# Kernel tuning notes

Hardware: AMD Instinct MI355X
Metric: run time of the kernel (lower is better)

## Reference

```python
import jax, jax.numpy as jnp
import numpy as np

N, IN_DIM, LAT, NB = 4096, 3000, 64, 2
SINKHORN_ITERS = 3


def _bce_logits(x, y):
    # torch BCEWithLogitsLoss, mean reduction, numerically stable
    return jnp.mean(jnp.maximum(x, 0.0) - x * y + jnp.log1p(jnp.exp(-jnp.abs(x))))


def _forward(feature_set, adj_set, graph_neigh_set, label_CSL_set, dist_mat_set,
             enc_W, dec_W, Ms, disc_W, disc_b, perm_idx):
    nb = feature_set.shape[0]
    hs = []
    loss_sl = 0.0
    loss_feat = 0.0
    for k in range(nb):  # small fixed loop over slices
        x, adj, mask, lab = feature_set[k], adj_set[k], graph_neigh_set[k], label_CSL_set[k]
        h = adj @ (x @ enc_W[k])            # GCN encode: spmm(adj, x @ W)
        out = adj @ (h @ dec_W[k])          # GCN decode
        x_a = x[perm_idx[k]]                # permutation(x): row shuffle
        h_a = adj @ (x_a @ enc_W[k])
        hr, har = jax.nn.relu(h), jax.nn.relu(h_a)

        def readout(emb):
            vsum = mask @ emb
            ge = vsum / mask.sum(1, keepdims=True)
            nrm = jnp.linalg.norm(ge, axis=1, keepdims=True)
            return ge / jnp.maximum(nrm, 1e-12)   # F.normalize p=2

        g = jax.nn.sigmoid(readout(hr))
        g_a = jax.nn.sigmoid(readout(har))

        def disc(c, hp, hm):
            s1 = jnp.einsum('nd,de,ne->n', hp, disc_W, c) + disc_b[0]
            s2 = jnp.einsum('nd,de,ne->n', hm, disc_W, c) + disc_b[0]
            return jnp.stack([s1, s2], axis=1)  # [N,2]

        ret = disc(g, hr, har)
        ret_a = disc(g_a, har, hr)
        loss_sl = loss_sl + _bce_logits(ret, lab) + _bce_logits(ret_a, lab)
        loss_feat = loss_feat + jnp.mean((x - out) ** 2)
        hs.append(h)

    loss_align = 0.0; loss_align_fix = 0.0; loss_maintain = 0.0
    loss_marginal = 0.0; loss_sparsity = 0.0
    for k in range(1, nb):
        src, tgt = hs[k - 1], hs[k]
        M = Ms[k - 1]
        m1, m2 = src.shape[0], tgt.shape[0]
        C = (src @ M) @ (tgt @ M).T / jnp.sqrt(jnp.float32(M.shape[0]))
        P = jax.nn.softmax(C, axis=1) / m1
        # NonSquareSinkhornKnopp.fit: alternate row/col normalization to uniform marginals
        for _ in range(SINKHORN_ITERS):
            P = P / (m1 * P.sum(1, keepdims=True))
            P = P / (m2 * P.sum(0, keepdims=True))
        cxy = P / P.sum(1, keepdims=True)
        cyx = P.T / P.T.sum(1, keepdims=True)
        # cdist(src, tgt)
        d2 = jnp.sum(src ** 2, 1)[:, None] + jnp.sum(tgt ** 2, 1)[None, :] - 2.0 * (src @ tgt.T)
        cd = jnp.sqrt(jnp.maximum(d2, 1e-12))
        loss_align = loss_align + jnp.sum(P * cd)
        f0, f1 = feature_set[k - 1], feature_set[k]
        loss_align_fix = loss_align_fix + jnp.mean((f0 - cxy @ f1) ** 2) + jnp.mean((f1 - cyx @ f0) ** 2)
        D0, D1 = dist_mat_set[k - 1], dist_mat_set[k]
        diff1 = D0 - cxy @ (D1 @ cxy.T)
        diff2 = D1 - cyx @ (D0 @ cyx.T)
        loss_maintain = loss_maintain + jnp.linalg.norm(diff1) / m1 + jnp.linalg.norm(diff2) / m2
        # replicate torch F.kl_div(input, target) = mean(target*(log target - input))
        p = jnp.full((m2,), 1.0 / m2, jnp.float32)
        q = P.sum(0)
        kld_pq = jnp.mean(q * (jnp.log(q) - p))
        kld_pp = jnp.mean(p * (jnp.log(p) - p))
        loss_marginal = loss_marginal + (kld_pq - kld_pp) * m2
        loss_sparsity = loss_sparsity - jnp.sum(P * jnp.log(P + 1e-10))
    return jnp.stack([loss_sl, loss_feat, loss_align, loss_align_fix,
                      loss_maintain, loss_marginal, loss_sparsity])


def setup_inputs():
    key = jax.random.key(0)
    ks = jax.random.split(key, 12)
    feature_set = jax.random.normal(ks[0], (NB, N, IN_DIM), jnp.float32)
    A = jax.random.uniform(ks[1], (NB, N, N), jnp.float32)
    adj_set = A / A.sum(-1, keepdims=True)  # row-stochastic dense stand-in for normalized sparse adj
    mask = (jax.random.uniform(ks[2], (NB, N, N)) < 0.01).astype(jnp.float32)
    graph_neigh_set = mask + jnp.eye(N, dtype=jnp.float32)[None]  # nonzero row sums
    lab = jnp.concatenate([jnp.ones((N, 1)), jnp.zeros((N, 1))], axis=1).astype(jnp.float32)
    label_CSL_set = jnp.broadcast_to(lab, (NB, N, 2))
    D = jax.random.uniform(ks[3], (NB, N, N), jnp.float32)
    dist_mat_set = 0.5 * (D + jnp.swapaxes(D, 1, 2))
    perm_idx = jnp.stack([jax.random.permutation(ks[4 + i], N) for i in range(NB)]).astype(jnp.int32)
    s_enc = np.float32(np.sqrt(2.0 / (IN_DIM + LAT)))
    enc_W = jax.random.normal(ks[6], (NB, IN_DIM, LAT), jnp.float32) * s_enc
    dec_W = jax.random.normal(ks[7], (NB, LAT, IN_DIM), jnp.float32) * s_enc
    s_lat = np.float32(np.sqrt(1.0 / LAT))
    Ms = jax.random.normal(ks[8], (NB - 1, LAT, LAT), jnp.float32) * s_lat
    disc_W = jax.random.normal(ks[9], (LAT, LAT), jnp.float32) * s_lat
    disc_b = jnp.zeros((1,), jnp.float32)
    return dict(feature_set=feature_set, adj_set=adj_set, graph_neigh_set=graph_neigh_set,
                label_CSL_set=label_CSL_set, dist_mat_set=dist_mat_set, perm_idx=perm_idx,
                enc_W=enc_W, dec_W=dec_W, Ms=Ms, disc_W=disc_W, disc_b=disc_b)


def reference(feature_set, adj_set, graph_neigh_set, label_CSL_set, dist_mat_set,
              perm_idx, enc_W, dec_W, Ms, disc_W, disc_b):
    return _forward(feature_set, adj_set, graph_neigh_set, label_CSL_set, dist_mat_set,
                    enc_W, dec_W, Ms, disc_W, disc_b, perm_idx)
```

## Files before the change

kernel.cpp:

```cpp
#include <hip/hip_runtime.h>
#include <cmath>

constexpr int kN   = 4096;
constexpr int kIN  = 3000;
constexpr int kINp = 3072;
constexpr int kLAT = 64;

enum { SL = 0, FEAT, ALN, FXA, FXB, SM1, SM2, SPS, NSLOT };

typedef __bf16 bf16x8 __attribute__((ext_vector_type(8)));
typedef float f32x4 __attribute__((ext_vector_type(4)));
typedef unsigned short u16x8 __attribute__((ext_vector_type(8)));
typedef unsigned short u16x4 __attribute__((ext_vector_type(4)));

template<bool IS_MAX>
__device__ __forceinline__ float blk_red(float v) {
  __shared__ float buf[4];
  #pragma unroll
  for (int s = 32; s > 0; s >>= 1) {
    float o = __shfl_down(v, s, 64);
    v = IS_MAX ? fmaxf(v, o) : (v + o);
  }
  int lane = threadIdx.x & 63, wv = threadIdx.x >> 6, nw = blockDim.x >> 6;
  __syncthreads();
  if (lane == 0) buf[wv] = v;
  __syncthreads();
  float r = buf[0];
  for (int i = 1; i < nw; i++) r = IS_MAX ? fmaxf(r, buf[i]) : (r + buf[i]);
  return r;
}

__device__ __forceinline__ float wave_red_sum(float v) {
  #pragma unroll
  for (int s = 32; s > 0; s >>= 1) v += __shfl_down(v, s, 64);
  return v;
}

__device__ __forceinline__ unsigned short f2bf(float f) {
  unsigned u = __builtin_bit_cast(unsigned, f);
  u += 0x7fffu + ((u >> 16) & 1u);
  return (unsigned short)(u >> 16);
}
__device__ __forceinline__ float bf2f(unsigned short h) {
  return __builtin_bit_cast(float, (unsigned)h << 16);
}

__device__ __forceinline__ void gload16(const unsigned short* g, unsigned short* l) {
  __builtin_amdgcn_global_load_lds(
      (const __attribute__((address_space(1))) unsigned int*)g,
      (__attribute__((address_space(3))) unsigned int*)l, 16, 0, 0);
}

template<int EPI, int XBF>
__global__ __launch_bounds__(256)
void bt_mfma_k(const unsigned short* __restrict__ A, const unsigned short* __restrict__ Bt,
               unsigned short* __restrict__ Cb, float* __restrict__ Cf,
               const void* __restrict__ Xv,
               const float* __restrict__ rowdiv, const float* __restrict__ coldiv,
               float* __restrict__ slot, int gx, int Nc, int K, int ldX, int sym)
{
  __shared__ unsigned short AB[3 * 8192];

  int orig = blockIdx.x;
  int bx, by;
  if (EPI == 2 && sym) {
    int x = orig & 7, i = orig >> 3;
    int u = x * 66 + i;
    float disc = 4225.f - 8.f * (float)u;
    by = (int)((65.f - sqrtf(fmaxf(disc, 0.f))) * 0.5f);
    while (by > 0 && 32 * by - by * (by - 1) / 2 > u) by--;
    while (32 * (by + 1) - (by + 1) * by / 2 <= u) by++;
    bx = by + (u - (32 * by - by * (by - 1) / 2));
  } else {
    int x = orig & 7, tt = orig >> 3;
    bx = tt >> 2;
    by = x * 4 + (tt & 3);
  }
  const int row0 = by * 128, col0 = bx * 128;

  const int t = threadIdx.x, l = t & 63, wv = t >> 6;
  const int wr = wv >> 1, wc = wv & 1;
  const int lr = l & 15, lkh = (l >> 4) << 3;

  f32x4 acc[4][4];
  #pragma unroll
  for (int i = 0; i < 4; i++)
    #pragma unroll
    for (int j = 0; j < 4; j++) acc[i][j] = (f32x4){0.f, 0.f, 0.f, 0.f};

  const int srow = l >> 2;
  const int sk   = (l & 3) << 3;
  const unsigned short* Ab = A  + (size_t)(row0 + srow) * K + sk;
  const unsigned short* Bb = Bt + (size_t)(col0 + srow) * K + sk;

  const int NT = K >> 5;

  auto STAGE = [&](int kt, int buf) {
    unsigned short* As = AB + buf * 8192;
    unsigned short* Bs = As + 4096;
    int k0 = kt << 5;
    #pragma unroll
    for (int h2 = 0; h2 < 2; h2++) {
      int c = wv * 2 + h2;
      gload16(Ab + (size_t)c * 16 * K + k0, As + c * 512);
      gload16(Bb + (size_t)c * 16 * K + k0, Bs + c * 512);
    }
  };

  STAGE(0, 0);
  if (NT > 1) STAGE(1, 1);
  if (NT > 2) STAGE(2, 2);
  int cur = 0;

  for (int kt = 0; kt < NT; ++kt) {
    int ahead = NT - 1 - kt;
    if (ahead >= 2)      { asm volatile("s_waitcnt vmcnt(8)" ::: "memory"); }
    else if (ahead == 1) { asm volatile("s_waitcnt vmcnt(4)" ::: "memory"); }
    else                 { asm volatile("s_waitcnt vmcnt(0)" ::: "memory"); }
    __builtin_amdgcn_sched_barrier(0);
    __builtin_amdgcn_s_barrier();

    const unsigned short* As = AB + cur * 8192;
    const unsigned short* Bs = As + 4096;
    u16x8 af[4], bfv[4];
    #pragma unroll
    for (int mi = 0; mi < 4; mi++)
      af[mi] = *(const u16x8*)&As[(wr * 64 + mi * 16 + lr) * 32 + lkh];
    #pragma unroll
    for (int ni = 0; ni < 4; ni++)
      bfv[ni] = *(const u16x8*)&Bs[(wc * 64 + ni * 16 + lr) * 32 + lkh];
    #pragma unroll
    for (int mi = 0; mi < 4; mi++)
      #pragma unroll
      for (int ni = 0; ni < 4; ni++)
        acc[mi][ni] = __builtin_amdgcn_mfma_f32_16x16x32_bf16(
            __builtin_bit_cast(bf16x8, af[mi]),
            __builtin_bit_cast(bf16x8, bfv[ni]), acc[mi][ni], 0, 0, 0);

    __builtin_amdgcn_s_barrier();
    if (kt + 3 < NT) STAGE(kt + 3, cur);
    cur = (cur == 2) ? 0 : cur + 1;
  }

  const int lcol = l & 15, lrow = (l >> 4) << 2;
  if (EPI == 0) {
    #pragma unroll
    for (int mi = 0; mi < 4; mi++) {
      int rr = row0 + wr * 64 + mi * 16 + lrow;
      #pragma unroll
      for (int ni = 0; ni < 4; ni++) {
        int cc = col0 + wc * 64 + ni * 16 + lcol;
        #pragma unroll
        for (int r = 0; r < 4; r++) {
          float v = acc[mi][ni][r];
          if (rowdiv) v /= rowdiv[rr + r];
          Cb[(size_t)(rr + r) * 4096 + cc] = f2bf(v);
        }
      }
    }
  } else if (EPI == 1) {
    #pragma unroll
    for (int mi = 0; mi < 4; mi++) {
      int rr = row0 + wr * 64 + mi * 16 + lrow;
      #pragma unroll
      for (int ni = 0; ni < 4; ni++) {
        int cc = col0 + wc * 64 + ni * 16 + lcol;
        #pragma unroll
        for (int r = 0; r < 4; r++)
          Cf[(size_t)(rr + r) * 4096 + cc] = acc[mi][ni][r];
      }
    }
  } else if (EPI == 2) {
    const float* Xf = (const float*)Xv;
    const unsigned short* Xh = (const unsigned short*)Xv;
    float part = 0.f;
    #pragma unroll
    for (int mi = 0; mi < 4; mi++) {
      int rr = row0 + wr * 64 + mi * 16 + lrow;
      #pragma unroll
      for (int ni = 0; ni < 4; ni++) {
        int cc = col0 + wc * 64 + ni * 16 + lcol;
        if (cc < Nc) {
          float cd = coldiv ? coldiv[cc] : 1.f;
          #pragma unroll
          for (int r = 0; r < 4; r++) {
            float v = acc[mi][ni][r];
            if (rowdiv) v /= rowdiv[rr + r];
            v /= cd;
            size_t xi = (size_t)(rr + r) * ldX + cc;
            float xval = XBF ? bf2f(Xh[xi]) : Xf[xi];
            float d = xval - v;
            part = fmaf(d, d, part);
          }
        }
      }
    }
    part = blk_red<false>(part);
    if (t == 0) {
      float wgt = (sym && col0 > row0) ? 2.f : 1.f;
      atomicAdd(slot, part * wgt);
    }
  } else {
    const unsigned short* Ph = (const unsigned short*)Xv;
    float a = 0.f, sp = 0.f;
    #pragma unroll
    for (int mi = 0; mi < 4; mi++) {
      int rr = row0 + wr * 64 + mi * 16 + lrow;
      #pragma unroll
      for (int ni = 0; ni < 4; ni++) {
        int cc = col0 + wc * 64 + ni * 16 + lcol;
        #pragma unroll
        for (int r = 0; r < 4; r++) {
          float g = acc[mi][ni][r];
          float p = bf2f(Ph[(size_t)(rr + r) * ldX + cc]);
          float d2 = rowdiv[rr + r] + coldiv[cc] - 2.f * g;
          a = fmaf(p, sqrtf(fmaxf(d2, 1e-12f)), a);
          sp = fmaf(p, logf(p + 1e-10f), sp);
        }
      }
    }
    a = blk_red<false>(a);
    sp = blk_red<false>(sp);
    if (t == 0) { atomicAdd(&slot[ALN], a); atomicAdd(&slot[SPS], sp); }
  }
}

__global__ __launch_bounds__(256)
void ns_mfma_k(const unsigned short* __restrict__ A, const unsigned short* __restrict__ Bt,
               float* __restrict__ C, int Nc, int K, int KC, int ldC)
{
  __shared__ unsigned short AB[2 * 8192];
  int ks = blockIdx.x & 15, strip = blockIdx.x >> 4;
  const int row0 = strip * 128;
  const int kbase = ks * KC;

  const int t = threadIdx.x, l = t & 63, wv = t >> 6;
  const int wr = wv >> 1, wc = wv & 1;
  const int lr = l & 15, lkh = (l >> 4) << 3;

  f32x4 acc[4][4];
  #pragma unroll
  for (int i = 0; i < 4; i++)
    #pragma unroll
    for (int j = 0; j < 4; j++) acc[i][j] = (f32x4){0.f, 0.f, 0.f, 0.f};

  const int srow = l >> 2;
  const int sk   = (l & 3) << 3;
  const unsigned short* Ab = A  + (size_t)(row0 + srow) * K + kbase + sk;
  const unsigned short* Bb = Bt + (size_t)srow * K + kbase + sk;

  const int NT = KC >> 5;

  auto STAGE = [&](int kt, int buf) {
    unsigned short* As = AB + buf * 8192;
    unsigned short* Bs = As + 4096;
    int k0 = kt << 5;
    #pragma unroll
    for (int h2 = 0; h2 < 2; h2++) {
      int c = wv * 2 + h2;
      gload16(Ab + (size_t)c * 16 * K + k0, As + c * 512);
      gload16(Bb + (size_t)c * 16 * K + k0, Bs + c * 512);
    }
  };

  STAGE(0, 0);
  if (NT > 1) STAGE(1, 1);
  int cur = 0;

  for (int kt = 0; kt < NT; ++kt) {
    if (kt + 1 < NT) { asm volatile("s_waitcnt vmcnt(4)" ::: "memory"); }
    else             { asm volatile("s_waitcnt vmcnt(0)" ::: "memory"); }
    __builtin_amdgcn_sched_barrier(0);
    __builtin_amdgcn_s_barrier();

    const unsigned short* As = AB + cur * 8192;
    const unsigned short* Bs = As + 4096;
    u16x8 af[4], bfv[4];
    #pragma unroll
    for (int mi = 0; mi < 4; mi++)
      af[mi] = *(const u16x8*)&As[(wr * 64 + mi * 16 + lr) * 32 + lkh];
    #pragma unroll
    for (int ni = 0; ni < 4; ni++)
      bfv[ni] = *(const u16x8*)&Bs[(wc * 64 + ni * 16 + lr) * 32 + lkh];
    #pragma unroll
    for (int mi = 0; mi < 4; mi++)
      #pragma unroll
      for (int ni = 0; ni < 4; ni++)
        acc[mi][ni] = __builtin_amdgcn_mfma_f32_16x16x32_bf16(
            __builtin_bit_cast(bf16x8, af[mi]),
            __builtin_bit_cast(bf16x8, bfv[ni]), acc[mi][ni], 0, 0, 0);

    __builtin_amdgcn_s_barrier();
    if (kt + 2 < NT) STAGE(kt + 2, cur);
    cur ^= 1;
  }

  const int lcol = l & 15, lrow = (l >> 4) << 2;
  #pragma unroll
  for (int mi = 0; mi < 4; mi++) {
    int rr = row0 + wr * 64 + mi * 16 + lrow;
    #pragma unroll
    for (int ni = 0; ni < 4; ni++) {
      int cc = wc * 64 + ni * 16 + lcol;
      if (cc < Nc) {
        #pragma unroll
        for (int r = 0; r < 4; r++)
          atomicAdd(&C[(size_t)(rr + r) * ldC + cc], acc[mi][ni][r]);
      }
    }
  }
}

__global__ void cvt_k(const float* __restrict__ s, unsigned short* __restrict__ d,
                      int n8, float scale)
{
  int i = blockIdx.x * 256 + threadIdx.x;
  if (i < n8) {
    float4 a = ((const float4*)s)[2 * i], b = ((const float4*)s)[2 * i + 1];
    u16x8 w;
    w[0] = f2bf(a.x * scale); w[1] = f2bf(a.y * scale);
    w[2] = f2bf(a.z * scale); w[3] = f2bf(a.w * scale);
    w[4] = f2bf(b.x * scale); w[5] = f2bf(b.y * scale);
    w[6] = f2bf(b.z * scale); w[7] = f2bf(b.w * scale);
    ((u16x8*)d)[i] = w;
  }
}

__global__ void cvt_pad_k(const float* __restrict__ s, unsigned short* __restrict__ d)
{
  int i = blockIdx.x * 256 + threadIdx.x;
  int row = i / 384, c8 = (i - row * 384) * 8;
  u16x8 w = (u16x8)0;
  if (c8 < kIN) {
    const float* sp = s + (size_t)row * kIN + c8;
    float4 a = *(const float4*)sp, b = *(const float4*)(sp + 4);
    w[0] = f2bf(a.x); w[1] = f2bf(a.y); w[2] = f2bf(a.z); w[3] = f2bf(a.w);
    w[4] = f2bf(b.x); w[5] = f2bf(b.y); w[6] = f2bf(b.z); w[7] = f2bf(b.w);
  }
  ((u16x8*)d)[i] = w;
}

__global__ void cvt_cols_k(const float* __restrict__ s, unsigned short* __restrict__ d)
{
  int i = blockIdx.x * 256 + threadIdx.x;
  int row = i >> 3, c8 = (i & 7) * 8;
  const float* sp = s + (size_t)row * 128 + c8;
  float4 a = *(const float4*)sp, b = *(const float4*)(sp + 4);
  u16x8 w;
  w[0] = f2bf(a.x); w[1] = f2bf(a.y); w[2] = f2bf(a.z); w[3] = f2bf(a.w);
  w[4] = f2bf(b.x); w[5] = f2bf(b.y); w[6] = f2bf(b.z); w[7] = f2bf(b.w);
  ((u16x8*)d)[i] = w;
}

template<bool RELU>
__global__ void tr_k(const float* __restrict__ src, unsigned short* __restrict__ dst,
                     int R, int C, int sld, int dld)
{
  __shared__ float tile[32][33];
  int c0 = blockIdx.x * 32, r0 = blockIdx.y * 32;
  int tr_ = threadIdx.x >> 3, tc4 = (threadIdx.x & 7) << 2;
  #pragma unroll
  for (int j = 0; j < 4; j++) {
    int r = r0 + tr_, c = c0 + tc4 + j;
    float v = (r < R && c < C) ? src[(size_t)r * sld + c] : 0.f;
    if (RELU) v = fmaxf(v, 0.f);
    tile[tr_][tc4 + j] = v;
  }
  __syncthreads();
  u16x4 wv;
  #pragma unroll
  for (int j = 0; j < 4; j++) wv[j] = f2bf(tile[tc4 + j][tr_]);
  *(u16x4*)&dst[(size_t)(c0 + tr_) * dld + r0 + tc4] = wv;
}

__global__ __launch_bounds__(256)
void gemm_small_k(const float* __restrict__ A, const float* __restrict__ B,
                  float* __restrict__ C, int M, int Nc, int K,
                  int ldA, int ldB, int ldC)
{
  __shared__ float As[16][68];
  __shared__ float Bs[16][68];
  int tid = threadIdx.x;
  int tx = tid & 15, ty = tid >> 4;
  int row0 = blockIdx.y * 64, col0 = blockIdx.x * 64;
  float acc[4][4] = {};

  for (int k0 = 0; k0 < K; k0 += 16) {
    {
      int m = tid >> 2, kk = (tid & 3) << 2;
      const float* ap = A + (size_t)(row0 + m) * ldA + k0 + kk;
      float4 v = *(const float4*)ap;
      As[kk + 0][m] = v.x; As[kk + 1][m] = v.y; As[kk + 2][m] = v.z; As[kk + 3][m] = v.w;
    }
    {
      int kk = tid >> 4, c = (tid & 15) << 2;
      const float* bp = B + (size_t)(k0 + kk) * ldB + col0 + c;
      #pragma unroll
      for (int i = 0; i < 4; i++)
        Bs[kk][c + i] = (col0 + c + i < Nc) ? bp[i] : 0.f;
    }
    __syncthreads();
    #pragma unroll
    for (int kk = 0; kk < 16; kk++) {
      float4 a4 = *(const float4*)&As[kk][ty << 2];
      float4 b4 = *(const float4*)&Bs[kk][tx << 2];
      float av[4] = {a4.x, a4.y, a4.z, a4.w};
      float bv[4] = {b4.x, b4.y, b4.z, b4.w};
      #pragma unroll
// ... 24 lines not shown
  int r0 = blockIdx.x * 8;
  float csl[16] = {};
  float cdiv[16];
  if (mode != 0) {
    #pragma unroll
    for (int t = 0; t < 4; t++) {
      float4 c4 = ((const float4*)cs_in)[tid + t * 256];
      cdiv[4 * t + 0] = 1.f / (4096.f * c4.x);
      cdiv[4 * t + 1] = 1.f / (4096.f * c4.y);
      cdiv[4 * t + 2] = 1.f / (4096.f * c4.z);
      cdiv[4 * t + 3] = 1.f / (4096.f * c4.w);
    }
  }
  for (int rr = 0; rr < 8; rr++) {
    int row = r0 + rr;
    float4* prow = (float4*)(P + (size_t)row * 4096);
    float4 r[4];
    #pragma unroll
    for (int t = 0; t < 4; t++) r[t] = prow[tid + t * 256];

    if (mode == 0) {
      float m = -3.4e38f;
      #pragma unroll
      for (int t = 0; t < 4; t++)
        m = fmaxf(m, fmaxf(fmaxf(r[t].x, r[t].y), fmaxf(r[t].z, r[t].w)));
      m = blk_red<true>(m);
      float s = 0.f;
      #pragma unroll
      for (int t = 0; t < 4; t++) {
        r[t].x = expf(r[t].x - m); r[t].y = expf(r[t].y - m);
        r[t].z = expf(r[t].z - m); r[t].w = expf(r[t].w - m);
        s += r[t].x + r[t].y + r[t].z + r[t].w;
      }
      s = blk_red<false>(s);
      float f = 1.f / (s * 4096.f);
      #pragma unroll
      for (int t = 0; t < 4; t++) {
        r[t].x *= f; r[t].y *= f; r[t].z *= f; r[t].w *= f;
        prow[tid + t * 256] = r[t];
        csl[4 * t + 0] += r[t].x; csl[4 * t + 1] += r[t].y;
        csl[4 * t + 2] += r[t].z; csl[4 * t + 3] += r[t].w;
      }
    } else {
      float s = 0.f;
      #pragma unroll
      for (int t = 0; t < 4; t++) {
        r[t].x *= cdiv[4 * t + 0]; r[t].y *= cdiv[4 * t + 1];
        r[t].z *= cdiv[4 * t + 2]; r[t].w *= cdiv[4 * t + 3];
        s += r[t].x + r[t].y + r[t].z + r[t].w;
      }
      s = blk_red<false>(s);
      if (mode == 1) {
        float f = 1.f / (4096.f * s);
        #pragma unroll
        for (int t = 0; t < 4; t++) {
          r[t].x *= f; r[t].y *= f; r[t].z *= f; r[t].w *= f;
          prow[tid + t * 256] = r[t];
          csl[4 * t + 0] += r[t].x; csl[4 * t + 1] += r[t].y;
          csl[4 * t + 2] += r[t].z; csl[4 * t + 3] += r[t].w;
        }
      } else {
        if (tid == 0) rs[row] = s;
        #pragma unroll
        for (int t = 0; t < 4; t++) {
          prow[tid + t * 256] = r[t];
          u16x4 w;
          w[0] = f2bf(r[t].x); w[1] = f2bf(r[t].y);
          w[2] = f2bf(r[t].z); w[3] = f2bf(r[t].w);
          *(u16x4*)&Pb[(size_t)row * 4096 + 4 * (tid + t * 256)] = w;
          csl[4 * t + 0] += r[t].x; csl[4 * t + 1] += r[t].y;
          csl[4 * t + 2] += r[t].z; csl[4 * t + 3] += r[t].w;
        }
      }
    }
  }
  #pragma unroll
  for (int t = 0; t < 4; t++) {
    int j = 4 * (tid + t * 256);
    atomicAdd(&cs_out[j + 0], csl[4 * t + 0]);
    atomicAdd(&cs_out[j + 1], csl[4 * t + 1]);
    atomicAdd(&cs_out[j + 2], csl[4 * t + 2]);
    atomicAdd(&cs_out[j + 3], csl[4 * t + 3]);
  }
}

__global__ __launch_bounds__(256)
void rowsum_k(const float* __restrict__ Pm, float* __restrict__ vec)
{
  int i = blockIdx.x, tid = threadIdx.x;
  const float4* prow = (const float4*)(Pm + (size_t)i * kN);
  float s = 0.f;
  #pragma unroll
  for (int t = 0; t < 4; t++) {
    float4 r = prow[tid + t * 256];
    s += r.x + r.y + r.z + r.w;
  }
  s = blk_red<false>(s);
  if (tid == 0) vec[i] = s;
}

__global__ void relu_k(const float* __restrict__ in, float* __restrict__ out, int n)
{
  int i = blockIdx.x * blockDim.x + threadIdx.x;
  if (i < n) out[i] = fmaxf(in[i], 0.f);
}

__global__ void gather_k(float* __restrict__ XP, const int* __restrict__ perm)
{
  int gid = blockIdx.x * 256 + threadIdx.x;
  int i = gid >> 6, j = gid & 63;
  XP[(size_t)i * 128 + 64 + j] = XP[(size_t)perm[i] * 128 + j];
}

__global__ void sqnorm_k(const float* __restrict__ H, int ld, float* __restrict__ outv)
{
  int gid = blockIdx.x * 256 + threadIdx.x;
  int row = gid >> 6, j = gid & 63;
  float v = H[(size_t)row * ld + j];
  float p = wave_red_sum(v * v);
  if (j == 0) outv[row] = p;
}

__global__ void readout_k(const float* __restrict__ vs2, const float* __restrict__ mrs,
                          float* __restrict__ g2)
{
  int q = blockIdx.x, j = threadIdx.x;
  float v = vs2[(size_t)q * 64 + j] / mrs[q >> 1];
  float p = v * v;
  #pragma unroll
  for (int s = 1; s < 64; s <<= 1) p += __shfl_xor(p, s, 64);
  float nrm = sqrtf(p);
  v = v / fmaxf(nrm, 1e-12f);
  g2[(size_t)q * 64 + j] = 1.f / (1.f + expf(-v));
}

__device__ __forceinline__ float bce_term(float x, float y) {
  return fmaxf(x, 0.f) - x * y + log1pf(expf(-fabsf(x)));
}

__global__ void disc_k(const float* __restrict__ G2, const float* __restrict__ W2,
                       const float* __restrict__ lab, const float* __restrict__ bptr,
                       float* __restrict__ acc)
{
  int i = blockIdx.x, j = threadIdx.x;
  float gj  = G2[(size_t)(2 * i) * 64 + j];
  float gaj = G2[(size_t)(2 * i + 1) * 64 + j];
  float hw  = W2[(size_t)(2 * i) * 64 + j];
  float haw = W2[(size_t)(2 * i + 1) * 64 + j];
  float s1 = hw * gj, s2 = haw * gj, s1a = haw * gaj, s2a = hw * gaj;
  #pragma unroll
  for (int s = 1; s < 64; s <<= 1) {
    s1  += __shfl_xor(s1, s, 64);
    s2  += __shfl_xor(s2, s, 64);
    s1a += __shfl_xor(s1a, s, 64);
    s2a += __shfl_xor(s2a, s, 64);
  }
  if (j == 0) {
    float b = bptr[0];
    float y0 = lab[i * 2 + 0], y1 = lab[i * 2 + 1];
    float t = bce_term(s1 + b, y0) + bce_term(s2 + b, y1)
            + bce_term(s1a + b, y0) + bce_term(s2a + b, y1);
    atomicAdd(&acc[SL], t);
  }
}

__global__ __launch_bounds__(256)
void finalize_k(const float* __restrict__ acc, const float* __restrict__ cs,
                float* __restrict__ out)
{
  int tid = threadIdx.x;
  float invm2 = 1.f / (float)kN;
  float t = 0.f;
  for (int j = tid; j < kN; j += 256) {
    float q = cs[j];
    t += q * (logf(q) - invm2);
  }
  t = blk_red<false>(t);
  if (tid == 0) {
    float kld_pq = t * invm2;
    float kld_pp = invm2 * (logf(invm2) - invm2);
    out[0] = acc[SL] / (2.f * (float)kN);
// ... 23 lines not shown
  const float* discW = (const float*)d_in[9];
  const float* discb = (const float*)d_in[10];
  float* out = (float*)d_out;

  const size_t SZNN = (size_t)kN * kN;

  char* cur = (char*)d_ws;
  auto alloc = [&](size_t bytes) {
    char* p = cur;
    cur += (bytes + 255) & ~(size_t)255;
    return p;
  };
  float* P            = (float*)alloc(SZNN * 4);
  unsigned short* Pb  = (unsigned short*)alloc(SZNN * 2);
  unsigned short* PbT = (unsigned short*)alloc(SZNN * 2);
  unsigned short* Db  = (unsigned short*)alloc(SZNN * 2);
  unsigned short* ajb = (unsigned short*)alloc(SZNN * 2);
  unsigned short* xb  = (unsigned short*)alloc((size_t)kN * kINp * 2);
  unsigned short* dWtb= (unsigned short*)alloc((size_t)kINp * kLAT * 2);
  unsigned short* ahb = (unsigned short*)alloc((size_t)kN * kLAT * 2);
  unsigned short* encWtp = (unsigned short*)alloc((size_t)128 * kINp * 2);
  unsigned short* XPt = (unsigned short*)alloc((size_t)128 * kN * 2);
  unsigned short* hbTp= (unsigned short*)alloc((size_t)128 * kN * 2);
  unsigned short* HRt = (unsigned short*)alloc((size_t)128 * kN * 2);
  unsigned short* smb = (unsigned short*)alloc((size_t)kN * kLAT * 2);
  unsigned short* tmb = (unsigned short*)alloc((size_t)kN * kLAT * 2);
  unsigned short* h0b = (unsigned short*)alloc((size_t)kN * kLAT * 2);
  unsigned short* h1b = (unsigned short*)alloc((size_t)kN * kLAT * 2);
  float* XP  = (float*)alloc((size_t)kN * 128 * 4);
  float* HH0 = (float*)alloc((size_t)kN * 128 * 4);
  float* HH1 = (float*)alloc((size_t)kN * 128 * 4);
  float* HR  = (float*)alloc((size_t)kN * 128 * 4);
  float* VS  = (float*)alloc((size_t)kN * 128 * 4);
  float* G2  = (float*)alloc((size_t)kN * 128 * 4);
  float* W2  = (float*)alloc((size_t)kN * 128 * 4);
  float* SM_ = (float*)alloc((size_t)kN * kLAT * 4);
  float* TM_ = (float*)alloc((size_t)kN * kLAT * 4);
  float* ah  = (float*)alloc((size_t)kN * kLAT * 4);
  float* sns = (float*)alloc(kN * 4);
  float* snt = (float*)alloc(kN * 4);
  float* rs  = (float*)alloc(kN * 4);
  float* cs  = (float*)alloc(kN * 4);
  float* csA = (float*)alloc(kN * 4);
  float* csB = (float*)alloc(kN * 4);
  float* mrs = (float*)alloc(kN * 4);
  float* acc = (float*)alloc(NSLOT * 4);

  unsigned short* Tb  = (unsigned short*)P;
  unsigned short* ftb = ajb;

  hipMemsetAsync(acc, 0, NSLOT * sizeof(float), stream);

  for (int k = 0; k < 2; k++) {
    const float* x    = feat  + (size_t)k * kN * kIN;
    const float* adj  = adjs  + (size_t)k * SZNN;
    const float* msk  = gmask + (size_t)k * SZNN;
    const float* lab  = labs  + (size_t)k * kN * 2;
    const int*   perm = perms + (size_t)k * kN;
    const float* eW   = encW  + (size_t)k * kIN * kLAT;
    const float* dW   = decW  + (size_t)k * kLAT * kIN;
    float* HHk = (k == 0) ? HH0 : HH1;

    cvt_pad_k<<<6144, 256, 0, stream>>>(x, xb);
    hipMemsetAsync(encWtp, 0, (size_t)128 * kINp * 2, stream);
    tr_k<false><<<dim3(2, (kIN + 31) / 32), 256, 0, stream>>>(eW, encWtp, kIN, kLAT, kLAT, kINp);
    hipMemsetAsync(XP, 0, (size_t)kN * 128 * 4, stream);
    ns_mfma_k<<<512, 256, 0, stream>>>(xb, encWtp, XP, kLAT, kINp, kINp / 16, 128);
    gather_k<<<kN * 64 / 256, 256, 0, stream>>>(XP, perm);
    tr_k<false><<<dim3(4, 128), 256, 0, stream>>>(XP, XPt, kN, 128, 128, kN);
    cvt_k<<<(int)(SZNN / 8 / 256), 256, 0, stream>>>(adj, ajb, (int)(SZNN / 8), 1.f);
    hipMemsetAsync(HHk, 0, (size_t)kN * 128 * 4, stream);
    ns_mfma_k<<<512, 256, 0, stream>>>(ajb, XPt, HHk, 128, kN, kN / 16, 128);
    hipMemsetAsync(hbTp, 0, (size_t)128 * kN * 2, stream);
    tr_k<false><<<dim3(2, 128), 256, 0, stream>>>(HHk, hbTp, kN, kLAT, 128, kN);
    hipMemsetAsync(ah, 0, (size_t)kN * kLAT * 4, stream);
    ns_mfma_k<<<512, 256, 0, stream>>>(ajb, hbTp, ah, kLAT, kN, kN / 16, kLAT);
    cvt_k<<<128, 256, 0, stream>>>(ah, ahb, kN * kLAT / 8, 1.f);
    tr_k<false><<<dim3(kINp / 32, 2), 256, 0, stream>>>(dW, dWtb, kLAT, kIN, kIN, kLAT);
    bt_mfma_k<2, 1><<<(kINp / 128) * 32, 256, 0, stream>>>(
        ahb, dWtb, nullptr, nullptr, xb, nullptr, nullptr, &acc[FEAT],
        kINp / 128, kIN, kLAT, kINp, 0);
    relu_k<<<kN * 128 / 256, 256, 0, stream>>>(HHk, HR, kN * 128);
    tr_k<true><<<dim3(4, 128), 256, 0, stream>>>(HHk, HRt, kN, 128, 128, kN);
    cvt_k<<<(int)(SZNN / 8 / 256), 256, 0, stream>>>(msk, ajb, (int)(SZNN / 8), 1.f);
    hipMemsetAsync(VS, 0, (size_t)kN * 128 * 4, stream);
    ns_mfma_k<<<512, 256, 0, stream>>>(ajb, HRt, VS, 128, kN, kN / 16, 128);
    rowsum_k<<<kN, 256, 0, stream>>>(msk, mrs);
    readout_k<<<2 * kN, 64, 0, stream>>>(VS, mrs, G2);
    gemm_small_k<<<dim3(1, 128), 256, 0, stream>>>(HR, discW, W2, 2 * kN, kLAT, kLAT,
                                                   kLAT, kLAT, kLAT);
    disc_k<<<kN, 64, 0, stream>>>(G2, W2, lab, discb, acc);
  }

  const float* f0 = feat;
  const float* f1 = feat + (size_t)kN * kIN;
  const float* D0 = dists;
  const float* D1 = dists + SZNN;

  gemm_small_k<<<dim3(1, 64), 256, 0, stream>>>(HH0, MsW, SM_, kN, kLAT, kLAT, 128, kLAT, kLAT);
  gemm_small_k<<<dim3(1, 64), 256, 0, stream>>>(HH1, MsW, TM_, kN, kLAT, kLAT, 128, kLAT, kLAT);
  cvt_k<<<128, 256, 0, stream>>>(SM_, smb, kN * kLAT / 8, 0.125f);
  cvt_k<<<128, 256, 0, stream>>>(TM_, tmb, kN * kLAT / 8, 1.f);
  bt_mfma_k<1, 0><<<1024, 256, 0, stream>>>(smb, tmb, nullptr, P, nullptr, nullptr, nullptr,
                                            nullptr, 32, kN, kLAT, 0, 0);

  hipMemsetAsync(csA, 0, kN * 4, stream);
  sink_k<<<512, 256, 0, stream>>>(P, nullptr, nullptr, csA, nullptr, 0);
  hipMemsetAsync(csB, 0, kN * 4, stream);
  sink_k<<<512, 256, 0, stream>>>(P, nullptr, csA, csB, nullptr, 1);
  hipMemsetAsync(csA, 0, kN * 4, stream);
  sink_k<<<512, 256, 0, stream>>>(P, nullptr, csB, csA, nullptr, 1);
  hipMemsetAsync(cs, 0, kN * 4, stream);
  sink_k<<<512, 256, 0, stream>>>(P, Pb, csA, cs, rs, 2);

  tr_k<false><<<dim3(kN / 32, kN / 32), 256, 0, stream>>>(P, PbT, kN, kN, kN, kN);

  cvt_cols_k<<<128, 256, 0, stream>>>(HH0, h0b);
  cvt_cols_k<<<128, 256, 0, stream>>>(HH1, h1b);
  sqnorm_k<<<kN * 64 / 256, 256, 0, stream>>>(HH0, 128, sns);
  sqnorm_k<<<kN * 64 / 256, 256, 0, stream>>>(HH1, 128, snt);
  bt_mfma_k<3, 1><<<1024, 256, 0, stream>>>(h0b, h1b, nullptr, nullptr, Pb, sns, snt, acc,
                                            32, kN, kLAT, kN, 0);

  tr_k<false><<<dim3(kINp / 32, kN / 32), 256, 0, stream>>>(f1, ftb, kN, kIN, kIN, kN);
  bt_mfma_k<2, 0><<<(kINp / 128) * 32, 256, 0, stream>>>(
      Pb, ftb, nullptr, nullptr, f0, rs, nullptr, &acc[FXA], kINp / 128, kIN, kN, kIN, 0);
  tr_k<false><<<dim3(kINp / 32, kN / 32), 256, 0, stream>>>(f0, ftb, kN, kIN, kIN, kN);
  bt_mfma_k<2, 0><<<(kINp / 128) * 32, 256, 0, stream>>>(
      PbT, ftb, nullptr, nullptr, f1, cs, nullptr, &acc[FXB], kINp / 128, kIN, kN, kIN, 0);

  cvt_k<<<(int)(SZNN / 8 / 256), 256, 0, stream>>>(D1, Db, (int)(SZNN / 8), 1.f);
  bt_mfma_k<0, 0><<<1024, 256, 0, stream>>>(Pb, Db, Tb, nullptr, nullptr, rs, nullptr,
                                            nullptr, 32, kN, kN, 0, 0);
  bt_mfma_k<2, 0><<<528, 256, 0, stream>>>(Tb, Pb, nullptr, nullptr, D0, nullptr, rs,
                                           &acc[SM1], 32, kN, kN, kN, 1);
  cvt_k<<<(int)(SZNN / 8 / 256), 256, 0, stream>>>(D0, Db, (int)(SZNN / 8), 1.f);
  bt_mfma_k<0, 0><<<1024, 256, 0, stream>>>(PbT, Db, Tb, nullptr, nullptr, cs, nullptr,
                                            nullptr, 32, kN, kN, 0, 0);
  bt_mfma_k<2, 0><<<528, 256, 0, stream>>>(Tb, PbT, nullptr, nullptr, D1, nullptr, cs,
                                           &acc[SM2], 32, kN, kN, kN, 1);

  finalize_k<<<1, 256, 0, stream>>>(acc, cs, out);
}
```

Measured before the change: 2.052 ms.

## Add 256x256-tile 8-wave MFMA GEMM kernel for large NxN and feature GEMMs

Adds a new bf16 MFMA GEMM kernel with 256x256 output tiles, 512 threads (8 waves), a 64-wide K step split into double-buffered phases, an XOR-swizzled LDS layout to avoid bank conflicts, and s_setprio around the MFMA bursts. The big P·D, T·P and P·F GEMMs now run on this kernel instead of the 128x128 triple-buffered one. The aim is more data reuse per global load and less LDS conflict on the dominant 4096^3-scale GEMMs. In exchange it uses 128KB of LDS and far fewer blocks, so occupancy and tail balance could suffer. The old kernel's unused epilogue and symmetric-tile paths are removed.

```diff
diff --git a/kernel.cpp b/kernel.cpp
--- a/kernel.cpp
+++ b/kernel.cpp
@@ -15,7 +15,7 @@
 
 template<bool IS_MAX>
 __device__ __forceinline__ float blk_red(float v) {
-  __shared__ float buf[4];
+  __shared__ float buf[8];
   #pragma unroll
   for (int s = 32; s > 0; s >>= 1) {
     float o = __shfl_down(v, s, 64);
@@ -51,6 +51,172 @@
       (__attribute__((address_space(3))) unsigned int*)l, 16, 0, 0);
 }
 
+#define VMW(n) asm volatile("s_waitcnt vmcnt(" #n ")" ::: "memory")
+
+template<int EPI, int XBF>
+__global__ __launch_bounds__(512, 2)
+void g8_mfma_k(const unsigned short* __restrict__ A, const unsigned short* __restrict__ Bt,
+               unsigned short* __restrict__ Cb, const void* __restrict__ Xv,
+               const float* __restrict__ rowdiv, const float* __restrict__ coldiv,
+               float* __restrict__ slot, int Nc, int K, int ldX, int sym)
+{
+  __shared__ unsigned short AB[65536];
+
+  int orig = blockIdx.x;
+  int bx, by;
+  if (EPI == 2 && sym) {
+    int x = orig & 7, i = orig >> 3;
+    int u = x * 17 + i;
+    by = 0; int cum = 0;
+    while (cum + (16 - by) <= u) { cum += 16 - by; by++; }
+    bx = by + (u - cum);
+  } else {
+    int x = orig & 7, tt = orig >> 3;
+    bx = tt >> 1; by = x * 2 + (tt & 1);
+  }
+  const int row0 = by * 256, col0 = bx * 256;
+
+  const int t = threadIdx.x, l = t & 63, wv = t >> 6;
+  const int wr = wv >> 2, wc = wv & 3;
+  const int lr = l & 15;
+  const int sA = (l >> 4) ^ ((lr >> 1) & 3);
+
+  f32x4 acc[8][4];
+  #pragma unroll
+  for (int i = 0; i < 8; i++)
+    #pragma unroll
+    for (int j = 0; j < 4; j++) acc[i][j] = (f32x4){0.f, 0.f, 0.f, 0.f};
+
+  const int NT = K >> 6;
+  const int NI = NT >> 1;
+
+  const int srow  = l >> 2;
+  const int sslot = (l & 3) ^ ((l >> 3) & 3);
+  const unsigned short* Ap = A  + (size_t)(row0 + srow) * K + sslot * 8;
+  const unsigned short* Bp = Bt + (size_t)(col0 + srow) * K + sslot * 8;
+
+  auto STG = [&](int tile, int r) {
+    if (tile >= NT) return;
+    int buf = tile & 1, ks = r >> 1;
+    const unsigned short* src = (r & 1) ? Bp : Ap;
+    unsigned short* dst = AB + buf * 32768 + r * 8192;
+    size_t koff = (size_t)tile * 64 + ks * 32;
+    #pragma unroll
+    for (int j = 0; j < 2; j++) {
+      int c = wv * 2 + j;
+      gload16(src + (size_t)c * 16 * K + koff, dst + c * 512);
+    }
+  };
+
+#define PHASE(WN, BUF, KS, NH, STILE, SR)                                      \
+  {                                                                            \
+    if ((WN) == 8) VMW(8); else if ((WN) == 6) VMW(6);                         \
+    else if ((WN) == 4) VMW(4); else if ((WN) == 0) VMW(0);                    \
+    __builtin_amdgcn_s_barrier();                                              \
+    u16x8 af[8], bfv[2];                                                       \
+    {                                                                          \
+      const unsigned short* ab = &AB[(BUF) * 32768 + (KS) * 16384];            \
+      _Pragma("unroll")                                                        \
+      for (int mi = 0; mi < 8; mi++)                                           \
+        af[mi] = *(const u16x8*)&ab[(wr * 128 + mi * 16 + lr) * 32 + sA * 8];  \
+      const unsigned short* bb = ab + 8192;                                    \
+      _Pragma("unroll")                                                        \
+      for (int nj = 0; nj < 2; nj++)                                           \
+        bfv[nj] = *(const u16x8*)&bb[(wc * 64 + (NH) * 32 + nj * 16 + lr) * 32 \
+                                     + sA * 8];                                \
+    }                                                                          \
+    if ((STILE) >= 0) STG(STILE, SR);                                          \
+    asm volatile("s_waitcnt lgkmcnt(0)" ::: "memory");                         \
+    __builtin_amdgcn_sched_barrier(0);                                         \
+    __builtin_amdgcn_s_setprio(1);                                             \
+    _Pragma("unroll")                                                          \
+    for (int mi = 0; mi < 8; mi++) {                                           \
+      acc[mi][(NH) * 2 + 0] = __builtin_amdgcn_mfma_f32_16x16x32_bf16(         \
+          __builtin_bit_cast(bf16x8, af[mi]),                                  \
+          __builtin_bit_cast(bf16x8, bfv[0]), acc[mi][(NH) * 2 + 0], 0, 0, 0); \
+      acc[mi][(NH) * 2 + 1] = __builtin_amdgcn_mfma_f32_16x16x32_bf16(         \
+          __builtin_bit_cast(bf16x8, af[mi]),                                  \
+          __builtin_bit_cast(bf16x8, bfv[1]), acc[mi][(NH) * 2 + 1], 0, 0, 0); \
+    }                                                                          \
+    __builtin_amdgcn_s_setprio(0);                                             \
+    __builtin_amdgcn_s_barrier();                                              \
+  }
+
+  STG(0, 0); STG(0, 1); STG(0, 2); STG(0, 3); STG(1, 0); STG(1, 1);
+
+  for (int i = 0; i < NI - 1; ++i) {
+    int T = 2 * i;
+    PHASE(8, 0, 0, 0, T + 1, 2);
+    PHASE(6, 0, 0, 1, T + 1, 3);
+    PHASE(-1, 0, 1, 0, T + 2, 0);
+    PHASE(-1, 0, 1, 1, T + 2, 1);
+    PHASE(8, 1, 0, 0, T + 2, 2);
+    PHASE(6, 1, 0, 1, T + 2, 3);
+    PHASE(-1, 1, 1, 0, T + 3, 0);
+    PHASE(-1, 1, 1, 1, T + 3, 1);
+  }
+  {
+    int T = 2 * (NI - 1);
+    PHASE(8, 0, 0, 0, T + 1, 2);
+    PHASE(6, 0, 0, 1, T + 1, 3);
+    PHASE(-1, 0, 1, 0, -1, 0);
+    PHASE(-1, 0, 1, 1, -1, 0);
+    PHASE(4, 1, 0, 0, -1, 0);
+    PHASE(0, 1, 0, 1, -1, 0);
+    PHASE(-1, 1, 1, 0, -1, 0);
+    PHASE(-1, 1, 1, 1, -1, 0);
+  }
+#undef PHASE
+
+  const int lcol = l & 15, lrow = (l >> 4) << 2;
+  if (EPI == 0) {
+    #pragma unroll
+    for (int mi = 0; mi < 8; mi++) {
+      int rr = row0 + wr * 128 + mi * 16 + lrow;
+      #pragma unroll
+      for (int nn = 0; nn < 4; nn++) {
+        int cc = col0 + wc * 64 + nn * 16 + lcol;
+        #pragma unroll
+        for (int r = 0; r < 4; r++) {
+          float v = acc[mi][nn][r];
+          if (rowdiv) v /= rowdiv[rr + r];
+          Cb[(size_t)(rr + r) * 4096 + cc] = f2bf(v);
+        }
+      }
+    }
+  } else {
+    const float* Xf = (const float*)Xv;
+    const unsigned short* Xh = (const unsigned short*)Xv;
+    float part = 0.f;
+    #pragma unroll
+    for (int mi = 0; mi < 8; mi++) {
+      int rr = row0 + wr * 128 + mi * 16 + lrow;
+      #pragma unroll
+      for (int nn = 0; nn < 4; nn++) {
+        int cc = col0 + wc * 64 + nn * 16 + lcol;
+        if (cc < Nc) {
+          float cd = coldiv ? coldiv[cc] : 1.f;
+          #pragma unroll
+          for (int r = 0; r < 4; r++) {
+            float v = acc[mi][nn][r];
+            if (rowdiv) v /= rowdiv[rr + r];
+            v /= cd;
+            size_t xi = (size_t)(rr + r) * ldX + cc;
+            float xval = XBF ? bf2f(Xh[xi]) : Xf[xi];
+            float d = xval - v;
+            part = fmaf(d, d, part);
+          }
+        }
+      }
+    }
+    part = blk_red<false>(part);
+    if (t == 0) {
+      float wgt = (sym && col0 > row0) ? 2.f : 1.f;
+      atomicAdd(slot, part * wgt);
+    }
+  }
+}
+
 template<int EPI, int XBF>
 __global__ __launch_bounds__(256)
 void bt_mfma_k(const unsigned short* __restrict__ A, const unsigned short* __restrict__ Bt,
@@ -62,20 +228,9 @@
   __shared__ unsigned short AB[3 * 8192];
 
   int orig = blockIdx.x;
-  int bx, by;
-  if (EPI == 2 && sym) {
-    int x = orig & 7, i = orig >> 3;
-    int u = x * 66 + i;
-    float disc = 4225.f - 8.f * (float)u;
-    by = (int)((65.f - sqrtf(fmaxf(disc, 0.f))) * 0.5f);
-    while (by > 0 && 32 * by - by * (by - 1) / 2 > u) by--;
-    while (32 * (by + 1) - (by + 1) * by / 2 <= u) by++;
-    bx = by + (u - (32 * by - by * (by - 1) / 2));
-  } else {
-    int x = orig & 7, tt = orig >> 3;
-    bx = tt >> 2;
-    by = x * 4 + (tt & 3);
-  }
+  int x = orig & 7, tt = orig >> 3;
+  int bx = tt >> 2;
+  int by = x * 4 + (tt & 3);
   const int row0 = by * 128, col0 = bx * 128;
 
   const int t = threadIdx.x, l = t & 63, wv = t >> 6;
@@ -114,9 +269,9 @@
 
   for (int kt = 0; kt < NT; ++kt) {
     int ahead = NT - 1 - kt;
-    if (ahead >= 2)      { asm volatile("s_waitcnt vmcnt(8)" ::: "memory"); }
-    else if (ahead == 1) { asm volatile("s_waitcnt vmcnt(4)" ::: "memory"); }
-    else                 { asm volatile("s_waitcnt vmcnt(0)" ::: "memory"); }
+    if (ahead >= 2)      { VMW(8); }
+    else if (ahead == 1) { VMW(4); }
+    else                 { VMW(0); }
     __builtin_amdgcn_sched_barrier(0);
     __builtin_amdgcn_s_barrier();
 
@@ -143,22 +298,7 @@
   }
 
   const int lcol = l & 15, lrow = (l >> 4) << 2;
-  if (EPI == 0) {
-    #pragma unroll
-    for (int mi = 0; mi < 4; mi++) {
-      int rr = row0 + wr * 64 + mi * 16 + lrow;
-      #pragma unroll
-      for (int ni = 0; ni < 4; ni++) {
-        int cc = col0 + wc * 64 + ni * 16 + lcol;
-        #pragma unroll
-        for (int r = 0; r < 4; r++) {
-          float v = acc[mi][ni][r];
-          if (rowdiv) v /= rowdiv[rr + r];
-          Cb[(size_t)(rr + r) * 4096 + cc] = f2bf(v);
-        }
-      }
-    }
-  } else if (EPI == 1) {
+  if (EPI == 1) {
     #pragma unroll
     for (int mi = 0; mi < 4; mi++) {
       int rr = row0 + wr * 64 + mi * 16 + lrow;
@@ -196,10 +336,7 @@
       }
     }
     part = blk_red<false>(part);
-    if (t == 0) {
-      float wgt = (sym && col0 > row0) ? 2.f : 1.f;
-      atomicAdd(slot, part * wgt);
-    }
+    if (t == 0) atomicAdd(slot, part);
   } else {
     const unsigned short* Ph = (const unsigned short*)Xv;
     float a = 0.f, sp = 0.f;
@@ -268,8 +405,8 @@
   int cur = 0;
 
   for (int kt = 0; kt < NT; ++kt) {
-    if (kt + 1 < NT) { asm volatile("s_waitcnt vmcnt(4)" ::: "memory"); }
-    else             { asm volatile("s_waitcnt vmcnt(0)" ::: "memory"); }
+    if (kt + 1 < NT) { VMW(4); }
+    else             { VMW(0); }
     __builtin_amdgcn_sched_barrier(0);
     __builtin_amdgcn_s_barrier();
 
@@ -759,22 +896,22 @@
                                             32, kN, kLAT, kN, 0);
 
   tr_k<false><<<dim3(kINp / 32, kN / 32), 256, 0, stream>>>(f1, ftb, kN, kIN, kIN, kN);
-  bt_mfma_k<2, 0><<<(kINp / 128) * 32, 256, 0, stream>>>(
-      Pb, ftb, nullptr, nullptr, f0, rs, nullptr, &acc[FXA], kINp / 128, kIN, kN, kIN, 0);
+  g8_mfma_k<2, 0><<<192, 512, 0, stream>>>(Pb, ftb, nullptr, f0, rs, nullptr,
+                                           &acc[FXA], kIN, kN, kIN, 0);
   tr_k<false><<<dim3(kINp / 32, kN / 32), 256, 0, stream>>>(f0, ftb, kN, kIN, kIN, kN);
-  bt_mfma_k<2, 0><<<(kINp / 128) * 32, 256, 0, stream>>>(
-      PbT, ftb, nullptr, nullptr, f1, cs, nullptr, &acc[FXB], kINp / 128, kIN, kN, kIN, 0);
+  g8_mfma_k<2, 0><<<192, 512, 0, stream>>>(PbT, ftb, nullptr, f1, cs, nullptr,
+                                           &acc[FXB], kIN, kN, kIN, 0);
 
   cvt_k<<<(int)(SZNN / 8 / 256), 256, 0, stream>>>(D1, Db, (int)(SZNN / 8), 1.f);
-  bt_mfma_k<0, 0><<<1024, 256, 0, stream>>>(Pb, Db, Tb, nullptr, nullptr, rs, nullptr,
-                                            nullptr, 32, kN, kN, 0, 0);
-  bt_mfma_k<2, 0><<<528, 256, 0, stream>>>(Tb, Pb, nullptr, nullptr, D0, nullptr, rs,
-                                           &acc[SM1], 32, kN, kN, kN, 1);
+  g8_mfma_k<0, 0><<<256, 512, 0, stream>>>(Pb, Db, Tb, nullptr, rs, nullptr,
+                                           nullptr, kN, kN, 0, 0);
+  g8_mfma_k<2, 0><<<136, 512, 0, stream>>>(Tb, Pb, nullptr, D0, nullptr, rs,
+                                           &acc[SM1], kN, kN, kN, 1);
   cvt_k<<<(int)(SZNN / 8 / 256), 256, 0, stream>>>(D0, Db, (int)(SZNN / 8), 1.f);
-  bt_mfma_k<0, 0><<<1024, 256, 0, stream>>>(PbT, Db, Tb, nullptr, nullptr, cs, nullptr,
-                                            nullptr, 32, kN, kN, 0, 0);
-  bt_mfma_k<2, 0><<<528, 256, 0, stream>>>(Tb, PbT, nullptr, nullptr, D1, nullptr, cs,
-                                           &acc[SM2], 32, kN, kN, kN, 1);
+  g8_mfma_k<0, 0><<<256, 512, 0, stream>>>(PbT, Db, Tb, nullptr, cs, nullptr,
+                                           nullptr, kN, kN, 0, 0);
+  g8_mfma_k<2, 0><<<136, 512, 0, stream>>>(Tb, PbT, nullptr, D1, nullptr, cs,
+                                           &acc[SM2], kN, kN, kN, 1);
 
   finalize_k<<<1, 256, 0, stream>>>(acc, cs, out);
 }
```

New measurement: 2.102 ms. 2.5% more time.

## Add 256x256-tile 8-wave MFMA GEMM for P@D and fuse mask rowsum into conversion

Applied to the files above, without the earlier changes.

Introduces a new bf16 MFMA GEMM kernel with 256x256 output tiles, 512 threads, swizzled LDS layout, double-buffered 64-wide K stages, split A/B phases and setprio. It replaces the 128x128 bt_mfma_k for the two 4096^3 P@D products. The larger tiles raise arithmetic intensity and cut redundant global loads. The mask row-sum is folded into the bf16 conversion pass using wave reductions and atomics, which removes a separate full read of the NxN mask. The cost is higher register and LDS pressure, and atomic float summation changes the order of additions.

```diff
diff --git a/kernel.cpp b/kernel.cpp
--- a/kernel.cpp
+++ b/kernel.cpp
@@ -15,7 +15,7 @@
 
 template<bool IS_MAX>
 __device__ __forceinline__ float blk_red(float v) {
-  __shared__ float buf[4];
+  __shared__ float buf[8];
   #pragma unroll
   for (int s = 32; s > 0; s >>= 1) {
     float o = __shfl_down(v, s, 64);
@@ -49,6 +49,150 @@
   __builtin_amdgcn_global_load_lds(
       (const __attribute__((address_space(1))) unsigned int*)g,
       (__attribute__((address_space(3))) unsigned int*)l, 16, 0, 0);
+}
+
+#define VMW(n) asm volatile("s_waitcnt vmcnt(" #n ")" ::: "memory")
+
+__global__ __launch_bounds__(512, 2)
+void g8_mfma_k(const unsigned short* __restrict__ A, const unsigned short* __restrict__ Bt,
+               unsigned short* __restrict__ Cb, const float* __restrict__ rowdiv, int K)
+{
+  __shared__ unsigned short AB[65536];
+
+  int orig = blockIdx.x;
+  int x = orig & 7, tt = orig >> 3;
+  int bx = tt >> 1, by = x * 2 + (tt & 1);
+  const int row0 = by * 256, col0 = bx * 256;
+
+  const int t = threadIdx.x, l = t & 63, wv = t >> 6;
+  const int wr = wv >> 2, wc = wv & 3;
+  const int lr = l & 15;
+  const int sA = (l >> 4) ^ ((lr >> 1) & 3);
+
+  f32x4 acc[8][4];
+  #pragma unroll
+  for (int i = 0; i < 8; i++)
+    #pragma unroll
+    for (int j = 0; j < 4; j++) acc[i][j] = (f32x4){0.f, 0.f, 0.f, 0.f};
+
+  const int NT = K >> 6;
+  const int NI = NT >> 1;
+
+  const int srow  = l >> 2;
+  const int sslot = (l & 3) ^ ((l >> 3) & 3);
+  const unsigned short* Ap = A  + (size_t)(row0 + srow) * K + sslot * 8;
+  const unsigned short* Bp = Bt + (size_t)(col0 + srow) * K + sslot * 8;
+
+  auto STG = [&](int tile, int r) {
+    if (tile >= NT) return;
+    int buf = tile & 1, ks = r >> 1;
+    const unsigned short* src = (r & 1) ? Bp : Ap;
+    unsigned short* dst = AB + buf * 32768 + r * 8192;
+    size_t koff = (size_t)tile * 64 + ks * 32;
+    #pragma unroll
+    for (int j = 0; j < 2; j++) {
+      int c = wv * 2 + j;
+      gload16(src + (size_t)c * 16 * K + koff, dst + c * 512);
+    }
+  };
+
+  u16x8 af[8], bfv[2];
+
+#define MFMA16(AV, BV, ACC) \
+  ACC = __builtin_amdgcn_mfma_f32_16x16x32_bf16( \
+      __builtin_bit_cast(bf16x8, AV), __builtin_bit_cast(bf16x8, BV), ACC, 0, 0, 0)
+
+#define PH_A(WN, BUF, KS, STILE, SR)                                           \
+  {                                                                            \
+    if ((WN) == 8) VMW(8); else if ((WN) == 4) VMW(4);                         \
+    else if ((WN) == 0) VMW(0);                                                \
+    __builtin_amdgcn_s_barrier();                                              \
+    {                                                                          \
+      const unsigned short* ab = &AB[(BUF) * 32768 + (KS) * 16384];            \
+      _Pragma("unroll")                                                        \
+      for (int mi = 0; mi < 8; mi++)                                           \
+        af[mi] = *(const u16x8*)&ab[(wr * 128 + mi * 16 + lr) * 32 + sA * 8];  \
+      const unsigned short* bb = ab + 8192;                                    \
+      bfv[0] = *(const u16x8*)&bb[(wc * 64 +  0 + lr) * 32 + sA * 8];          \
+      bfv[1] = *(const u16x8*)&bb[(wc * 64 + 16 + lr) * 32 + sA * 8];          \
+    }                                                                          \
+    if ((STILE) >= 0) STG(STILE, SR);                                          \
+    asm volatile("s_waitcnt lgkmcnt(0)" ::: "memory");                         \
+    __builtin_amdgcn_sched_barrier(0);                                         \
+    __builtin_amdgcn_s_setprio(1);                                             \
+    _Pragma("unroll")                                                          \
+    for (int mi = 0; mi < 8; mi++) {                                           \
+      MFMA16(af[mi], bfv[0], acc[mi][0]);                                      \
+      MFMA16(af[mi], bfv[1], acc[mi][1]);                                      \
+    }                                                                          \
+    __builtin_amdgcn_s_setprio(0);                                             \
+    __builtin_amdgcn_s_barrier();                                              \
+  }
+
+#define PH_B(BUF, KS, STILE, SR)                                               \
+  {                                                                            \
+    __builtin_amdgcn_s_barrier();                                              \
+    {                                                                          \
+      const unsigned short* bb = &AB[(BUF) * 32768 + (KS) * 16384 + 8192];     \
+      bfv[0] = *(const u16x8*)&bb[(wc * 64 + 32 + lr) * 32 + sA * 8];          \
+      bfv[1] = *(const u16x8*)&bb[(wc * 64 + 48 + lr) * 32 + sA * 8];          \
+    }                                                                          \
+    if ((STILE) >= 0) STG(STILE, SR);                                          \
+    asm volatile("s_waitcnt lgkmcnt(0)" ::: "memory");                         \
+    __builtin_amdgcn_sched_barrier(0);                                         \
+    __builtin_amdgcn_s_setprio(1);                                             \
+    _Pragma("unroll")                                                          \
+    for (int mi = 0; mi < 8; mi++) {                                           \
+      MFMA16(af[mi], bfv[0], acc[mi][2]);                                      \
+      MFMA16(af[mi], bfv[1], acc[mi][3]);                                      \
+    }                                                                          \
+    __builtin_amdgcn_s_setprio(0);                                             \
+    __builtin_amdgcn_s_barrier();                                              \
+  }
+
+  STG(0, 0); STG(0, 1); STG(0, 2); STG(0, 3); STG(1, 0); STG(1, 1);
+
+  for (int i = 0; i < NI - 1; ++i) {
+    int T = 2 * i;
+    PH_A(8, 0, 0, T + 1, 2);
+    PH_B(   0, 0, T + 1, 3);
+    PH_A(8, 0, 1, T + 2, 0);
+    PH_B(   0, 1, T + 2, 1);
+    PH_A(8, 1, 0, T + 2, 2);
+    PH_B(   1, 0, T + 2, 3);
+    PH_A(8, 1, 1, T + 3, 0);
+    PH_B(   1, 1, T + 3, 1);
+  }
+  {
+    int T = 2 * (NI - 1);
+    PH_A(8, 0, 0, T + 1, 2);
+    PH_B(   0, 0, T + 1, 3);
+    PH_A(8, 0, 1, -1, 0);
+    PH_B(   0, 1, -1, 0);
+    PH_A(4, 1, 0, -1, 0);
+    PH_B(   1, 0, -1, 0);
+    PH_A(0, 1, 1, -1, 0);
+    PH_B(   1, 1, -1, 0);
+  }
+#undef PH_A
+#undef PH_B
+#undef MFMA16
+
+  const int lcol = l & 15, lrow = (l >> 4) << 2;
+  #pragma unroll
+  for (int mi = 0; mi < 8; mi++) {
+    int rr = row0 + wr * 128 + mi * 16 + lrow;
+    #pragma unroll
+    for (int nn = 0; nn < 4; nn++) {
+      int cc = col0 + wc * 64 + nn * 16 + lcol;
+      #pragma unroll
+      for (int r = 0; r < 4; r++) {
+        float v = acc[mi][nn][r];
+        if (rowdiv) v /= rowdiv[rr + r];
+        Cb[(size_t)(rr + r) * 4096 + cc] = f2bf(v);
+      }
+    }
+  }
 }
 
 template<int EPI, int XBF>
@@ -114,9 +258,9 @@
 
   for (int kt = 0; kt < NT; ++kt) {
     int ahead = NT - 1 - kt;
-    if (ahead >= 2)      { asm volatile("s_waitcnt vmcnt(8)" ::: "memory"); }
-    else if (ahead == 1) { asm volatile("s_waitcnt vmcnt(4)" ::: "memory"); }
-    else                 { asm volatile("s_waitcnt vmcnt(0)" ::: "memory"); }
+    if (ahead >= 2)      { VMW(8); }
+    else if (ahead == 1) { VMW(4); }
+    else                 { VMW(0); }
     __builtin_amdgcn_sched_barrier(0);
     __builtin_amdgcn_s_barrier();
 
@@ -143,22 +287,7 @@
   }
 
   const int lcol = l & 15, lrow = (l >> 4) << 2;
-  if (EPI == 0) {
-    #pragma unroll
-    for (int mi = 0; mi < 4; mi++) {
-      int rr = row0 + wr * 64 + mi * 16 + lrow;
-      #pragma unroll
-      for (int ni = 0; ni < 4; ni++) {
-        int cc = col0 + wc * 64 + ni * 16 + lcol;
-        #pragma unroll
-        for (int r = 0; r < 4; r++) {
-          float v = acc[mi][ni][r];
-          if (rowdiv) v /= rowdiv[rr + r];
-          Cb[(size_t)(rr + r) * 4096 + cc] = f2bf(v);
-        }
-      }
-    }
-  } else if (EPI == 1) {
+  if (EPI == 1) {
     #pragma unroll
     for (int mi = 0; mi < 4; mi++) {
       int rr = row0 + wr * 64 + mi * 16 + lrow;
@@ -268,8 +397,8 @@
   int cur = 0;
 
   for (int kt = 0; kt < NT; ++kt) {
-    if (kt + 1 < NT) { asm volatile("s_waitcnt vmcnt(4)" ::: "memory"); }
-    else             { asm volatile("s_waitcnt vmcnt(0)" ::: "memory"); }
+    if (kt + 1 < NT) { VMW(4); }
+    else             { VMW(0); }
     __builtin_amdgcn_sched_barrier(0);
     __builtin_amdgcn_s_barrier();
 
@@ -324,6 +453,20 @@
     w[6] = f2bf(b.z * scale); w[7] = f2bf(b.w * scale);
     ((u16x8*)d)[i] = w;
   }
+}
+
+__global__ void cvt_rs_k(const float* __restrict__ s, unsigned short* __restrict__ d,
+                         float* __restrict__ mrs)
+{
+  int i = blockIdx.x * 256 + threadIdx.x;
+  float4 a = ((const float4*)s)[2 * i], b = ((const float4*)s)[2 * i + 1];
+  u16x8 w;
+  w[0] = f2bf(a.x); w[1] = f2bf(a.y); w[2] = f2bf(a.z); w[3] = f2bf(a.w);
+  w[4] = f2bf(b.x); w[5] = f2bf(b.y); w[6] = f2bf(b.z); w[7] = f2bf(b.w);
+  ((u16x8*)d)[i] = w;
+  float s8 = a.x + a.y + a.z + a.w + b.x + b.y + b.z + b.w;
+  float ws = wave_red_sum(s8);
+  if ((threadIdx.x & 63) == 0) atomicAdd(&mrs[i >> 9], ws);
 }
 
 __global__ void cvt_pad_k(const float* __restrict__ s, unsigned short* __restrict__ d)
@@ -514,21 +657,6 @@
     atomicAdd(&cs_out[j + 2], csl[4 * t + 2]);
     atomicAdd(&cs_out[j + 3], csl[4 * t + 3]);
   }
-}
-
-__global__ __launch_bounds__(256)
-void rowsum_k(const float* __restrict__ Pm, float* __restrict__ vec)
-{
-  int i = blockIdx.x, tid = threadIdx.x;
-  const float4* prow = (const float4*)(Pm + (size_t)i * kN);
-  float s = 0.f;
-  #pragma unroll
-  for (int t = 0; t < 4; t++) {
-    float4 r = prow[tid + t * 256];
-    s += r.x + r.y + r.z + r.w;
-  }
-  s = blk_red<false>(s);
-  if (tid == 0) vec[i] = s;
 }
 
 __global__ void relu_k(const float* __restrict__ in, float* __restrict__ out, int n)
@@ -718,10 +846,10 @@
         kINp / 128, kIN, kLAT, kINp, 0);
     relu_k<<<kN * 128 / 256, 256, 0, stream>>>(HHk, HR, kN * 128);
     tr_k<true><<<dim3(4, 128), 256, 0, stream>>>(HHk, HRt, kN, 128, 128, kN);
-    cvt_k<<<(int)(SZNN / 8 / 256), 256, 0, stream>>>(msk, ajb, (int)(SZNN / 8), 1.f);
+    hipMemsetAsync(mrs, 0, kN * 4, stream);
+    cvt_rs_k<<<(int)(SZNN / 8 / 256), 256, 0, stream>>>(msk, ajb, mrs);
     hipMemsetAsync(VS, 0, (size_t)kN * 128 * 4, stream);
     ns_mfma_k<<<512, 256, 0, stream>>>(ajb, HRt, VS, 128, kN, kN / 16, 128);
-    rowsum_k<<<kN, 256, 0, stream>>>(msk, mrs);
     readout_k<<<2 * kN, 64, 0, stream>>>(VS, mrs, G2);
     gemm_small_k<<<dim3(1, 128), 256, 0, stream>>>(HR, discW, W2, 2 * kN, kLAT, kLAT,
                                                    kLAT, kLAT, kLAT);
@@ -766,13 +894,11 @@
       PbT, ftb, nullptr, nullptr, f1, cs, nullptr, &acc[FXB], kINp / 128, kIN, kN, kIN, 0);
 
   cvt_k<<<(int)(SZNN / 8 / 256), 256, 0, stream>>>(D1, Db, (int)(SZNN / 8), 1.f);
-  bt_mfma_k<0, 0><<<1024, 256, 0, stream>>>(Pb, Db, Tb, nullptr, nullptr, rs, nullptr,
-                                            nullptr, 32, kN, kN, 0, 0);
+  g8_mfma_k<<<256, 512, 0, stream>>>(Pb, Db, Tb, rs, kN);
   bt_mfma_k<2, 0><<<528, 256, 0, stream>>>(Tb, Pb, nullptr, nullptr, D0, nullptr, rs,
                                            &acc[SM1], 32, kN, kN, kN, 1);
   cvt_k<<<(int)(SZNN / 8 / 256), 256, 0, stream>>>(D0, Db, (int)(SZNN / 8), 1.f);
-  bt_mfma_k<0, 0><<<1024, 256, 0, stream>>>(PbT, Db, Tb, nullptr, nullptr, cs, nullptr,
-                                            nullptr, 32, kN, kN, 0, 0);
+  g8_mfma_k<<<256, 512, 0, stream>>>(PbT, Db, Tb, cs, kN);
   bt_mfma_k<2, 0><<<528, 256, 0, stream>>>(Tb, PbT, nullptr, nullptr, D1, nullptr, cs,
                                            &acc[SM2], 32, kN, kN, kN, 1);
 
```

New measurement: 2.061 ms. Within noise of the previous version (+0.4%).
